# Performance work log

Measured on AMD Instinct MI355X. Metric: run time of the kernel, lower is better.

The kernel has to match this reference:

```python
import jax, jax.numpy as jnp
import numpy as np

HIDDEN = 512
TEMPERATURE = float(np.sqrt(HIDDEN))  # scaled-dot temperature
BATCH = 64


def _build_weights(attn_weight, N, K):
    """Vectorized version of get_attn_weight: (S,S,H) with S = N*K+1.
    Regions: 0=same_sample, 1=same_class, 2=diff_class, 3=support->query,
    4=query->support, 5=query->query. Replicates the torch overwrite order."""
    S = N * K + 1
    NK = N * K
    i = jnp.arange(S)[:, None]
    j = jnp.arange(S)[None, :]
    idx = jnp.full((S, S), 2, dtype=jnp.int32)                      # w_diff_class
    idx = jnp.where((i // K) == (j // K), 1, idx)                   # w_same_class
    idx = jnp.where((i < NK) & (j == NK), 3, idx)                   # w_stoquery
    idx = jnp.where(i == j, 0, idx)                                 # w_same_sample (diag)
    idx = jnp.where((i == NK) & (j < NK), 4, idx)                   # w_querytos
    idx = jnp.where((i == NK) & (j == NK), 5, idx)                  # w_query
    return attn_weight[idx]  # (S, S, H)


def setup_inputs() -> dict:
    key = jax.random.key(0)
    kq, kk, kv, kw = jax.random.split(key, 4)
    N, K = 10, 10
    S = N * K + 1  # 101
    q = jax.random.normal(kq, (BATCH, S, HIDDEN), dtype=jnp.float32)
    k = jax.random.normal(kk, (BATCH, S, HIDDEN), dtype=jnp.float32)
    v = jax.random.normal(kv, (BATCH, S, HIDDEN), dtype=jnp.float32)
    bound = float(np.sqrt(6 / 2))
    attn_weight = jax.random.uniform(kw, (6, HIDDEN), dtype=jnp.float32,
                                     minval=-bound, maxval=bound)
    return {"q": q, "k": k, "v": v, "attn_weight": attn_weight, "N": N, "K": K}


def reference(q, k, v, attn_weight, N, K):
    # attn[b,i,j] = softmax_j(q.k^T / temperature)
    scores = jnp.einsum("bih,bjh->bij", q, k) / TEMPERATURE
    attn = jax.nn.softmax(scores, axis=2)  # dropout p=0 (eval) -> identity
    weights = _build_weights(attn_weight, N, K)  # (S,S,H)
    # out[b,i,h] = sum_j attn[b,i,j] * weights[i,j,h] * v[b,j,h]
    out = jnp.einsum("bij,ijh,bjh->bih", attn, weights, v)
    return out, attn
```

## Files before the change

kernel.cpp:

```cpp
#include <hip/hip_runtime.h>
#include <math.h>
#include <stdint.h>

#define BATCH 64
#define SEQ   101
#define HID   512
#define NKQ   100
#define KCLS  10
#define INV_TEMP 0.04419417382415922f

typedef short bf16x8 __attribute__((ext_vector_type(8)));
typedef float f32x4  __attribute__((ext_vector_type(4)));

__device__ inline void split_bf16(float x, short& hi, short& lo) {
    uint32_t u = __builtin_bit_cast(uint32_t, x);
    hi = (short)(u >> 16);
    float hf = __builtin_bit_cast(float, u & 0xFFFF0000u);
    float l  = x - hf;
    lo = (short)(__builtin_bit_cast(uint32_t, l) >> 16);
}
__device__ inline short rtn_bf16(float x) {
    uint32_t u = __builtin_bit_cast(uint32_t, x);
    return (short)((u + 0x7FFFu + ((u >> 16) & 1u)) >> 16);
}

#define KCH 64
#define KST 72

__global__ __launch_bounds__(512, 4)
void qk_softmax(const float* __restrict__ q, const float* __restrict__ k,
                float* __restrict__ attn, float* __restrict__ apad) {
    __shared__ short khi[128][KST];
    __shared__ short qhi[16][KST];
    __shared__ short qlo[16][KST];
    __shared__ float sc[16][132];
    const int b   = blockIdx.x & 63;
    const int i0  = (blockIdx.x >> 6) * 16;
    const int tid = threadIdx.x;
    const int wv  = tid >> 6, lane = tid & 63;
    const int m   = lane & 15;
    const int kq  = (lane >> 4) * 8;
    const int rq  = (lane >> 4) * 4;
    const int j0w = wv * 16;

    const float* qb = q + (size_t)b * SEQ * HID;
    const float* kb = k + (size_t)b * SEQ * HID;

    f32x4 acc = {};
    for (int kc = 0; kc < HID; kc += KCH) {
        #pragma unroll
        for (int s = 0; s < 4; ++s) {
            const int f = tid + s * 512;
            const int r = f >> 4, c = (f & 15) << 2;
            float4 x = make_float4(0.f, 0.f, 0.f, 0.f);
            if (r < SEQ) x = *(const float4*)(kb + (size_t)r * HID + kc + c);
            short4 hv;
            hv.x = rtn_bf16(x.x); hv.y = rtn_bf16(x.y);
            hv.z = rtn_bf16(x.z); hv.w = rtn_bf16(x.w);
            *(short4*)&khi[r][c] = hv;
        }
        if (tid < 256) {
            const int r = tid >> 4, c = (tid & 15) << 2;
            const int gi = i0 + r;
            float4 x = make_float4(0.f, 0.f, 0.f, 0.f);
            if (gi < SEQ) x = *(const float4*)(qb + (size_t)gi * HID + kc + c);
            short4 hv, lv;
            split_bf16(x.x, hv.x, lv.x);
            split_bf16(x.y, hv.y, lv.y);
            split_bf16(x.z, hv.z, lv.z);
            split_bf16(x.w, hv.w, lv.w);
            *(short4*)&qhi[r][c] = hv;
            *(short4*)&qlo[r][c] = lv;
        }
        __syncthreads();
        #pragma unroll
        for (int ks = 0; ks < KCH; ks += 32) {
            const bf16x8 qH = *(const bf16x8*)&qhi[m][ks + kq];
            const bf16x8 qL = *(const bf16x8*)&qlo[m][ks + kq];
            const bf16x8 kH = *(const bf16x8*)&khi[j0w + m][ks + kq];
            acc = __builtin_amdgcn_mfma_f32_16x16x32_bf16(qH, kH, acc, 0, 0, 0);
            acc = __builtin_amdgcn_mfma_f32_16x16x32_bf16(qL, kH, acc, 0, 0, 0);
        }
        __syncthreads();
    }
    #pragma unroll
    for (int r = 0; r < 4; ++r)
        sc[rq + r][j0w + m] = acc[r];
    __syncthreads();

    {
        const int row = tid >> 5, t32 = tid & 31;
        const int gi  = i0 + row;
        float mx = -1e30f;
        for (int j = t32; j < SEQ; j += 32) {
            float s = sc[row][j] * INV_TEMP;
            sc[row][j] = s;
            mx = fmaxf(mx, s);
        }
        #pragma unroll
        for (int off = 1; off < 32; off <<= 1) mx = fmaxf(mx, __shfl_xor(mx, off));
        float sum = 0.f;
        for (int j = t32; j < SEQ; j += 32) {
            float e = __expf(sc[row][j] - mx);
            sc[row][j] = e;
            sum += e;
        }
        #pragma unroll
        for (int off = 1; off < 32; off <<= 1) sum += __shfl_xor(sum, off);
        const float inv = 1.f / sum;
        if (gi < SEQ) {
            float* arow = attn + ((size_t)b * SEQ + gi) * SEQ;
            float* prow = apad + ((size_t)b * SEQ + gi) * 128;
            for (int j = t32; j < SEQ; j += 32) {
                float a = sc[row][j] * inv;
                arow[j] = a;
                prow[j] = a;
            }
            for (int j = SEQ + t32; j < 128; j += 32) prow[j] = 0.f;
        }
    }
}

#define VR 36
#define VT 144

__global__ __launch_bounds__(512, 6)
void pv_out(const float* __restrict__ v, const float* __restrict__ aw,
            const float* __restrict__ apad, float* __restrict__ out) {
    __shared__ float vraw[SEQ][VR];
    __shared__ short vth[32][VT];
    __shared__ short vtl[32][VT];
    const int b   = blockIdx.x & 63;
    const int h0  = (blockIdx.x >> 6) * 32;
    const int tid = threadIdx.x;
    const int wv  = tid >> 6, lane = tid & 63;
    const int m   = lane & 15;
    const int kq  = (lane >> 4) * 8;
    const int rq  = (lane >> 4) * 4;

    const float* vb = v + (size_t)b * SEQ * HID + h0;
    for (int f = tid; f < SEQ * 8; f += 512) {
        int r = f >> 3, c = (f & 7) << 2;
        *(float4*)&vraw[r][c] = *(const float4*)(vb + (size_t)r * HID + c);
    }
    __syncthreads();
    for (int it2 = tid; it2 < 32 * 36; it2 += 512) {
        int h = it2 & 31, j = (it2 >> 5) << 2;
        short4 hv, lv;
        split_bf16(j + 0 < SEQ ? vraw[j + 0][h] : 0.f, hv.x, lv.x);
        split_bf16(j + 1 < SEQ ? vraw[j + 1][h] : 0.f, hv.y, lv.y);
        split_bf16(j + 2 < SEQ ? vraw[j + 2][h] : 0.f, hv.z, lv.z);
        split_bf16(j + 3 < SEQ ? vraw[j + 3][h] : 0.f, hv.w, lv.w);
        *(short4*)&vth[h][j] = hv;
        *(short4*)&vtl[h][j] = lv;
    }
    __syncthreads();

    if (wv < 7) {
        const int i0 = wv * 16;
        int ai = i0 + m; if (ai > NKQ) ai = NKQ;
        const int ci = ai / KCLS;
        const float* ar = apad + ((size_t)b * SEQ + ai) * 128 + kq;
        f32x4 T[2] = {}, U[2] = {};
        #pragma unroll
        for (int ks = 0; ks < 4; ++ks) {
            float4 u0 = *(const float4*)(ar + ks * 32);
            float4 u1 = *(const float4*)(ar + ks * 32 + 4);
            float x[8] = {u0.x,u0.y,u0.z,u0.w,u1.x,u1.y,u1.z,u1.w};
            bf16x8 Ah, Al, Mh;
            #pragma unroll
            for (int e = 0; e < 8; ++e) {
                short h, l; split_bf16(x[e], h, l);
                Ah[e] = h; Al[e] = l;
                const int j = ks * 32 + kq + e;
                Mh[e] = ((j / KCLS) == ci) ? h : (short)0;
            }
            #pragma unroll
            for (int ht = 0; ht < 2; ++ht) {
                const bf16x8 Bh = *(const bf16x8*)&vth[ht * 16 + m][ks * 32 + kq];
                const bf16x8 Bl = *(const bf16x8*)&vtl[ht * 16 + m][ks * 32 + kq];
                T[ht] = __builtin_amdgcn_mfma_f32_16x16x32_bf16(Ah, Bh, T[ht], 0, 0, 0);
                T[ht] = __builtin_amdgcn_mfma_f32_16x16x32_bf16(Ah, Bl, T[ht], 0, 0, 0);
                T[ht] = __builtin_amdgcn_mfma_f32_16x16x32_bf16(Al, Bh, T[ht], 0, 0, 0);
                U[ht] = __builtin_amdgcn_mfma_f32_16x16x32_bf16(Mh, Bh, U[ht], 0, 0, 0);
            }
        }
        const float* ap = apad + (size_t)b * SEQ * 128;
        #pragma unroll
        for (int ht = 0; ht < 2; ++ht) {
            const int hl = ht * 16 + m;
            const int h  = h0 + hl;
            const float w0 = aw[0 * HID + h], w1 = aw[1 * HID + h], w2 = aw[2 * HID + h];
            const float w3 = aw[3 * HID + h], w4 = aw[4 * HID + h], w5 = aw[5 * HID + h];
            const float vN = vraw[NKQ][hl];
            #pragma unroll
            for (int r = 0; r < 4; ++r) {
                const int i = i0 + rq + r;
                if (i >= SEQ) continue;
                const float t = T[ht][r], u = U[ht][r];
                const float aiN = ap[(size_t)i * 128 + NKQ];
                float o;
                if (i < NKQ) {
                    const float aii = ap[(size_t)i * 128 + i];
                    const float vi  = vraw[i][hl];
                    o = w2 * t + (w1 - w2) * u + (w0 - w1) * aii * vi + (w3 - w2) * aiN * vN;
                } else {
                    o = w4 * t + (w5 - w4) * aiN * vN;
                }
                out[((size_t)b * SEQ + i) * HID + h] = o;
            }
        }
    }
}

extern "C" void kernel_launch(void* const* d_in, const int* in_sizes, int n_in,
                              void* d_out, int out_size, void* d_ws, size_t ws_size,
                              hipStream_t stream) {
    const float* q  = (const float*)d_in[0];
    const float* k  = (const float*)d_in[1];
    const float* v  = (const float*)d_in[2];
    const float* aw = (const float*)d_in[3];
    float* out  = (float*)d_out;
    float* attn = out + (size_t)BATCH * SEQ * HID;
    float* apad = (float*)d_ws;

    qk_softmax<<<dim3(448), dim3(512), 0, stream>>>(q, k, attn, apad);
    pv_out<<<dim3(1024), dim3(512), 0, stream>>>(v, aw, apad, out);
}
```

Before: 116.5 us.

## Fuse QK-softmax and PV kernels into one attention kernel with shared pool

Merges the two kernels into one. Each block keeps its 16-row attention tile in shared memory and streams V in 128-column chunks through a shared pool that is reused for the K tile, so the padded attention buffer no longer makes a round trip through global memory. This also removes a launch. In exchange, the grid is only 448 blocks, and each block now reads the full V for its batch, so V is loaded 7 times across the row tiles. The V staging also adds more barriers.

```diff
diff --git a/kernel.cpp b/kernel.cpp
--- a/kernel.cpp
+++ b/kernel.cpp
@@ -26,14 +26,28 @@
 
 #define KCH 64
 #define KST 72
+#define VST 72
+#define VRS 132
+
+#define OFF_QHI 18432
+#define OFF_QLO 20736
+#define OFF_VTH 33792
+#define OFF_VTL 52224
+#define POOLSZ  70656
 
 __global__ __launch_bounds__(512, 4)
-void qk_softmax(const float* __restrict__ q, const float* __restrict__ k,
-                float* __restrict__ attn, float* __restrict__ apad) {
-    __shared__ short khi[128][KST];
-    __shared__ short qhi[16][KST];
-    __shared__ short qlo[16][KST];
-    __shared__ float sc[16][132];
+void fused_attn(const float* __restrict__ q, const float* __restrict__ k,
+                const float* __restrict__ v, const float* __restrict__ aw,
+                float* __restrict__ out, float* __restrict__ attn) {
+    __shared__ __align__(16) char pool[POOLSZ];
+    __shared__ __align__(16) float sc[16][132];
+    short (*khi)[KST]  = (short(*)[KST])(pool);
+    short (*qhi)[KST]  = (short(*)[KST])(pool + OFF_QHI);
+    short (*qlo)[KST]  = (short(*)[KST])(pool + OFF_QLO);
+    float (*vraw)[VRS] = (float(*)[VRS])(pool);
+    short (*vth)[VST]  = (short(*)[VST])(pool + OFF_VTH);
+    short (*vtl)[VST]  = (short(*)[VST])(pool + OFF_VTL);
+
     const int b   = blockIdx.x & 63;
     const int i0  = (blockIdx.x >> 6) * 16;
     const int tid = threadIdx.x;
@@ -45,6 +59,7 @@
 
     const float* qb = q + (size_t)b * SEQ * HID;
     const float* kb = k + (size_t)b * SEQ * HID;
+    const float* vb = v + (size_t)b * SEQ * HID;
 
     f32x4 acc = {};
     for (int kc = 0; kc < HID; kc += KCH) {
@@ -108,107 +123,101 @@
         #pragma unroll
         for (int off = 1; off < 32; off <<= 1) sum += __shfl_xor(sum, off);
         const float inv = 1.f / sum;
-        if (gi < SEQ) {
-            float* arow = attn + ((size_t)b * SEQ + gi) * SEQ;
-            float* prow = apad + ((size_t)b * SEQ + gi) * 128;
-            for (int j = t32; j < SEQ; j += 32) {
-                float a = sc[row][j] * inv;
-                arow[j] = a;
-                prow[j] = a;
-            }
-            for (int j = SEQ + t32; j < 128; j += 32) prow[j] = 0.f;
-        }
-    }
-}
-
-#define VR 36
-#define VT 144
-
-__global__ __launch_bounds__(512, 6)
-void pv_out(const float* __restrict__ v, const float* __restrict__ aw,
-            const float* __restrict__ apad, float* __restrict__ out) {
-    __shared__ float vraw[SEQ][VR];
-    __shared__ short vth[32][VT];
-    __shared__ short vtl[32][VT];
-    const int b   = blockIdx.x & 63;
-    const int h0  = (blockIdx.x >> 6) * 32;
-    const int tid = threadIdx.x;
-    const int wv  = tid >> 6, lane = tid & 63;
-    const int m   = lane & 15;
-    const int kq  = (lane >> 4) * 8;
-    const int rq  = (lane >> 4) * 4;
-
-    const float* vb = v + (size_t)b * SEQ * HID + h0;
-    for (int f = tid; f < SEQ * 8; f += 512) {
-        int r = f >> 3, c = (f & 7) << 2;
-        *(float4*)&vraw[r][c] = *(const float4*)(vb + (size_t)r * HID + c);
+        float* arow = attn + ((size_t)b * SEQ + gi) * SEQ;
+        for (int j = t32; j < SEQ; j += 32) {
+            float a = sc[row][j] * inv;
+            sc[row][j] = a;
+            if (gi < SEQ) arow[j] = a;
+        }
+        for (int j = SEQ + t32; j < 128; j += 32) sc[row][j] = 0.f;
     }
     __syncthreads();
-    for (int it2 = tid; it2 < 32 * 36; it2 += 512) {
-        int h = it2 & 31, j = (it2 >> 5) << 2;
-        short4 hv, lv;
-        split_bf16(j + 0 < SEQ ? vraw[j + 0][h] : 0.f, hv.x, lv.x);
-        split_bf16(j + 1 < SEQ ? vraw[j + 1][h] : 0.f, hv.y, lv.y);
-        split_bf16(j + 2 < SEQ ? vraw[j + 2][h] : 0.f, hv.z, lv.z);
-        split_bf16(j + 3 < SEQ ? vraw[j + 3][h] : 0.f, hv.w, lv.w);
-        *(short4*)&vth[h][j] = hv;
-        *(short4*)&vtl[h][j] = lv;
-    }
-    __syncthreads();
-
-    if (wv < 7) {
-        const int i0 = wv * 16;
-        int ai = i0 + m; if (ai > NKQ) ai = NKQ;
-        const int ci = ai / KCLS;
-        const float* ar = apad + ((size_t)b * SEQ + ai) * 128 + kq;
-        f32x4 T[2] = {}, U[2] = {};
-        #pragma unroll
-        for (int ks = 0; ks < 4; ++ks) {
-            float4 u0 = *(const float4*)(ar + ks * 32);
-            float4 u1 = *(const float4*)(ar + ks * 32 + 4);
-            float x[8] = {u0.x,u0.y,u0.z,u0.w,u1.x,u1.y,u1.z,u1.w};
-            bf16x8 Ah, Al, Mh;
+
+    int ai = i0 + m; if (ai > NKQ) ai = NKQ;
+    const int ci = ai / KCLS;
+    uint32_t mbits = 0;
+    #pragma unroll
+    for (int ks = 0; ks < 4; ++ks)
+        #pragma unroll
+        for (int e = 0; e < 8; ++e)
+            if (((ks * 32 + kq + e) / KCLS) == ci) mbits |= (1u << (ks * 8 + e));
+    bf16x8 Ah[4], Al[4];
+    #pragma unroll
+    for (int ks = 0; ks < 4; ++ks) {
+        const f32x4 u0 = *(const f32x4*)&sc[m][ks * 32 + kq];
+        const f32x4 u1 = *(const f32x4*)&sc[m][ks * 32 + kq + 4];
+        const float x[8] = {u0[0], u0[1], u0[2], u0[3], u1[0], u1[1], u1[2], u1[3]};
+        #pragma unroll
+        for (int e = 0; e < 8; ++e) {
+            short h, l; split_bf16(x[e], h, l);
+            Ah[ks][e] = h; Al[ks][e] = l;
+        }
+    }
+
+    for (int hc = 0; hc < 4; ++hc) {
+        const int hbase = hc << 7;
+        f32x4 T = {}, U = {};
+        #pragma unroll
+        for (int half = 0; half < 2; ++half) {
+            __syncthreads();
             #pragma unroll
-            for (int e = 0; e < 8; ++e) {
-                short h, l; split_bf16(x[e], h, l);
-                Ah[e] = h; Al[e] = l;
-                const int j = ks * 32 + kq + e;
-                Mh[e] = ((j / KCLS) == ci) ? h : (short)0;
-            }
+            for (int s = 0; s < 4; ++s) {
+                const int f = tid + s * 512;
+                const int j = f >> 5, h4 = (f & 31) << 2;
+                const int jg = half * 64 + j;
+                float4 x = make_float4(0.f, 0.f, 0.f, 0.f);
+                if (jg < SEQ) x = *(const float4*)(vb + (size_t)jg * HID + hbase + h4);
+                *(float4*)&vraw[j][h4] = x;
+            }
+            __syncthreads();
             #pragma unroll
-            for (int ht = 0; ht < 2; ++ht) {
-                const bf16x8 Bh = *(const bf16x8*)&vth[ht * 16 + m][ks * 32 + kq];
-                const bf16x8 Bl = *(const bf16x8*)&vtl[ht * 16 + m][ks * 32 + kq];
-                T[ht] = __builtin_amdgcn_mfma_f32_16x16x32_bf16(Ah, Bh, T[ht], 0, 0, 0);
-                T[ht] = __builtin_amdgcn_mfma_f32_16x16x32_bf16(Ah, Bl, T[ht], 0, 0, 0);
-                T[ht] = __builtin_amdgcn_mfma_f32_16x16x32_bf16(Al, Bh, T[ht], 0, 0, 0);
-                U[ht] = __builtin_amdgcn_mfma_f32_16x16x32_bf16(Mh, Bh, U[ht], 0, 0, 0);
-            }
-        }
-        const float* ap = apad + (size_t)b * SEQ * 128;
-        #pragma unroll
-        for (int ht = 0; ht < 2; ++ht) {
-            const int hl = ht * 16 + m;
-            const int h  = h0 + hl;
-            const float w0 = aw[0 * HID + h], w1 = aw[1 * HID + h], w2 = aw[2 * HID + h];
-            const float w3 = aw[3 * HID + h], w4 = aw[4 * HID + h], w5 = aw[5 * HID + h];
-            const float vN = vraw[NKQ][hl];
+            for (int s = 0; s < 4; ++s) {
+                const int it = tid + s * 512;
+                const int h = it & 127, jl = (it >> 7) << 2;
+                short4 hv, lv;
+                split_bf16(vraw[jl + 0][h], hv.x, lv.x);
+                split_bf16(vraw[jl + 1][h], hv.y, lv.y);
+                split_bf16(vraw[jl + 2][h], hv.z, lv.z);
+                split_bf16(vraw[jl + 3][h], hv.w, lv.w);
+                *(short4*)&vth[h][jl] = hv;
+                *(short4*)&vtl[h][jl] = lv;
+            }
+            __syncthreads();
             #pragma unroll
-            for (int r = 0; r < 4; ++r) {
-                const int i = i0 + rq + r;
-                if (i >= SEQ) continue;
-                const float t = T[ht][r], u = U[ht][r];
-                const float aiN = ap[(size_t)i * 128 + NKQ];
-                float o;
-                if (i < NKQ) {
-                    const float aii = ap[(size_t)i * 128 + i];
-                    const float vi  = vraw[i][hl];
-                    o = w2 * t + (w1 - w2) * u + (w0 - w1) * aii * vi + (w3 - w2) * aiN * vN;
-                } else {
-                    o = w4 * t + (w5 - w4) * aiN * vN;
-                }
-                out[((size_t)b * SEQ + i) * HID + h] = o;
-            }
+            for (int ksl = 0; ksl < 2; ++ksl) {
+                const int ks = half * 2 + ksl;
+                const bf16x8 Bh = *(const bf16x8*)&vth[j0w + m][ksl * 32 + kq];
+                const bf16x8 Bl = *(const bf16x8*)&vtl[j0w + m][ksl * 32 + kq];
+                bf16x8 Mh;
+                #pragma unroll
+                for (int e = 0; e < 8; ++e)
+                    Mh[e] = (mbits & (1u << (ks * 8 + e))) ? Ah[ks][e] : (short)0;
+                T = __builtin_amdgcn_mfma_f32_16x16x32_bf16(Ah[ks], Bh, T, 0, 0, 0);
+                T = __builtin_amdgcn_mfma_f32_16x16x32_bf16(Ah[ks], Bl, T, 0, 0, 0);
+                T = __builtin_amdgcn_mfma_f32_16x16x32_bf16(Al[ks], Bh, T, 0, 0, 0);
+                U = __builtin_amdgcn_mfma_f32_16x16x32_bf16(Mh,     Bh, U, 0, 0, 0);
+            }
+        }
+        const int h = hbase + j0w + m;
+        const float w0 = aw[0 * HID + h], w1 = aw[1 * HID + h], w2 = aw[2 * HID + h];
+        const float w3 = aw[3 * HID + h], w4 = aw[4 * HID + h], w5 = aw[5 * HID + h];
+        const float vN = vb[(size_t)NKQ * HID + h];
+        #pragma unroll
+        for (int r = 0; r < 4; ++r) {
+            const int i = i0 + rq + r;
+            if (i >= SEQ) continue;
+            const int il = rq + r;
+            const float t = T[r], u = U[r];
+            const float aiN = sc[il][NKQ];
+            float o;
+            if (i < NKQ) {
+                const float aii = sc[il][i];
+                const float vi  = vb[(size_t)i * HID + h];
+                o = w2 * t + (w1 - w2) * u + (w0 - w1) * aii * vi + (w3 - w2) * aiN * vN;
+            } else {
+                o = w4 * t + (w5 - w4) * aiN * vN;
+            }
+            out[((size_t)b * SEQ + i) * HID + h] = o;
         }
     }
 }
@@ -222,8 +231,7 @@
     const float* aw = (const float*)d_in[3];
     float* out  = (float*)d_out;
     float* attn = out + (size_t)BATCH * SEQ * HID;
-    float* apad = (float*)d_ws;
-
-    qk_softmax<<<dim3(448), dim3(512), 0, stream>>>(q, k, attn, apad);
-    pv_out<<<dim3(1024), dim3(512), 0, stream>>>(v, aw, apad, out);
-}
+    (void)d_ws; (void)ws_size;
+
+    fused_attn<<<dim3(448), dim3(512), 0, stream>>>(q, k, v, aw, out, attn);
+}
```

Measured after the change: 122.8 us. 5.3% more time.
